# Performance work log

Hardware: AMD Instinct MI355X
Metric: run time of the kernel (lower is better)

The kernel has to match this reference:

```python
import jax, jax.numpy as jnp
import numpy as np

N_NODES = 100000
N_EDGES = 1600000
DK = 32
OUT_DIM = 32


def setup_inputs() -> dict:
    key = jax.random.key(0)
    ks = jax.random.split(key, 7)
    X = jax.random.normal(ks[0], (N_NODES, DK), dtype=jnp.float32)
    K = jax.random.normal(ks[1], (N_NODES, DK), dtype=jnp.float32)
    V = jax.random.normal(ks[2], (N_NODES, DK), dtype=jnp.float32)
    # output projection (nn.Dense(out_dim)) params
    W_o = jax.random.normal(ks[3], (DK, OUT_DIM), dtype=jnp.float32) / np.sqrt(DK)
    b_o = jnp.zeros((OUT_DIM,), dtype=jnp.float32)
    # sparsity descriptor td: edge list, dst sorted so segment ops see sorted ids
    src = jax.random.randint(ks[4], (N_EDGES,), 0, N_NODES, dtype=jnp.int32)
    dst = jnp.sort(jax.random.randint(ks[5], (N_EDGES,), 0, N_NODES, dtype=jnp.int32))
    return {"X": X, "K": K, "V": V, "W_o": W_o, "b_o": b_o,
            "src": src, "dst": dst, "num_seg": N_NODES}


def reference(X, K, V, W_o, b_o, src, dst, num_seg):
    dk = X.shape[-1]
    # per-edge attention logits: <Q[dst], K[src]> / dk  -> (E,)
    scores = jnp.einsum('ed,ed->e', jnp.take(X, dst, axis=0),
                        jnp.take(K, src, axis=0)) / dk
    # segment (per-neighborhood) softmax over edges sharing a dst node
    seg_max = jax.ops.segment_max(scores, dst, num_segments=num_seg,
                                  indices_are_sorted=True)
    e = jnp.exp(scores - jnp.take(seg_max, dst))
    denom = jax.ops.segment_sum(e, dst, num_segments=num_seg,
                                indices_are_sorted=True)
    alpha = e / jnp.take(denom, dst)  # (E,)
    # weighted aggregation of values, scattered back to nodes -> (N, dk)
    agg = jax.ops.segment_sum(alpha[:, None] * jnp.take(V, src, axis=0), dst,
                              num_segments=num_seg, indices_are_sorted=True)
    # output projection W_o
    return agg @ W_o + b_o
```

## Files before the change

### kernel.cpp

```cpp
#include <hip/hip_runtime.h>
#include <math.h>

#define DK 32
#define OUT_DIM 32

typedef float    f32x4 __attribute__((ext_vector_type(4)));
typedef _Float16 h2    __attribute__((ext_vector_type(2)));
typedef _Float16 h8    __attribute__((ext_vector_type(8)));

#if __has_builtin(__builtin_amdgcn_fdot2)
#define FDOT2(a, b, c) __builtin_amdgcn_fdot2((a), (b), (c), false)
#else
#define FDOT2(a, b, c) ((c) + (float)(a).x * (float)(b).x + (float)(a).y * (float)(b).y)
#endif

#if __has_builtin(__builtin_amdgcn_exp2f)
#define EXP2F(x) __builtin_amdgcn_exp2f(x)
#else
#define EXP2F(x) exp2f(x)
#endif

__device__ __forceinline__ h2 as_h2(unsigned u) {
    union { unsigned u; h2 h; } v; v.u = u; return v.h;
}
__device__ __forceinline__ unsigned as_u32(h2 h) {
    union { unsigned u; h2 h; } v; v.h = h; return v.u;
}
__device__ __forceinline__ h2 shfl_xor_h2(h2 v, int m) {
    union { unsigned u; h2 h; } x; x.h = v;
    x.u = (unsigned)__shfl_xor((int)x.u, m);
    return x.h;
}

__global__ void prep_kernel(const int* __restrict__ dst,
                            const float4* __restrict__ K4,
                            const float4* __restrict__ V4,
                            int E, int N,
                            int* __restrict__ row_ptr,
                            uint4* __restrict__ KVH) {
    const int t  = blockIdx.x * blockDim.x + threadIdx.x;
    const int e0 = t * 4;
    if (e0 < E) {
        int cur[4];
        if (e0 + 4 <= E) {
            const int4 dd = *(const int4*)(dst + e0);
            cur[0] = dd.x; cur[1] = dd.y; cur[2] = dd.z; cur[3] = dd.w;
        } else {
#pragma unroll
            for (int k = 0; k < 4; ++k)
                cur[k] = (e0 + k < E) ? dst[e0 + k] : 0;
        }
        int prev = (e0 == 0) ? -1 : dst[e0 - 1];
#pragma unroll
        for (int k = 0; k < 4; ++k) {
            const int ee = e0 + k;
            if (ee < E) {
                for (int j = prev + 1; j <= cur[k]; ++j) row_ptr[j] = ee;
                if (ee == E - 1)
                    for (int j = cur[k] + 1; j <= N; ++j) row_ptr[j] = E;
                prev = cur[k];
            }
        }
    }
    if (t < N * 8) {
        const float4 kf = K4[t];
        const float4 vf = V4[t];
        h2 k01, k23, v01, v23;
        k01.x = (_Float16)kf.x;  k01.y = (_Float16)kf.y;
        k23.x = (_Float16)kf.z;  k23.y = (_Float16)kf.w;
        v01.x = (_Float16)vf.x;  v01.y = (_Float16)vf.y;
        v23.x = (_Float16)vf.z;  v23.y = (_Float16)vf.w;
        uint4 o;
        o.x = as_u32(k01); o.y = as_u32(k23); o.z = as_u32(v01); o.w = as_u32(v23);
        KVH[t] = o;
    }
}

__global__ void build_row_ptr_kernel(const int* __restrict__ dst, int E, int N,
                                     int* __restrict__ row_ptr) {
    int e = blockIdx.x * blockDim.x + threadIdx.x;
    if (e >= E) return;
    int cur  = dst[e];
    int prev = (e == 0) ? -1 : dst[e - 1];
    for (int j = prev + 1; j <= cur; ++j) row_ptr[j] = e;
    if (e == E - 1) {
        for (int j = cur + 1; j <= N; ++j) row_ptr[j] = E;
    }
}

__global__ __launch_bounds__(256) void gat_fused_kernel(
    const float* __restrict__ X, const uint4* __restrict__ KV,
    const float* __restrict__ Wo, const float* __restrict__ bo,
    const int* __restrict__ src, const int* __restrict__ row_ptr,
    float* __restrict__ out, int N) {

    __shared__ uint4 s_part[16 * 17];

    const int tid  = threadIdx.x;
    const int w    = tid >> 6;
    const int lane = tid & 63;
    const int g    = lane >> 3;
    const int c    = lane & 7;

    const int n_blk = blockIdx.x * 16;
    const int n_w   = n_blk + w * 4;

    const int rpv = row_ptr[min(n_w + min(lane, 4), N)];

    const float4* X4 = (const float4*)X;
    unsigned* part32 = (unsigned*)s_part;
    const float scale = 0.03125f * 1.44269504f;

    int beg[4], en[4], cap[4], e[4];
#pragma unroll
    for (int i = 0; i < 4; ++i) {
        beg[i] = __builtin_amdgcn_readlane(rpv, i);
        en[i]  = __builtin_amdgcn_readlane(rpv, i + 1);
        cap[i] = max(en[i] - 1, 0);
        e[i]   = beg[i];
    }

    h2 q01[4], q23[4];
#pragma unroll
    for (int i = 0; i < 4; ++i) {
        const float4 qf = X4[min(n_w + i, N - 1) * 8 + c];
        q01[i].x = (_Float16)(qf.x * scale);
        q01[i].y = (_Float16)(qf.y * scale);
        q23[i].x = (_Float16)(qf.z * scale);
        q23[i].y = (_Float16)(qf.w * scale);
    }

    float l[4] = {0.0f, 0.0f, 0.0f, 0.0f};
    h2 a01[4], a23[4];
#pragma unroll
    for (int i = 0; i < 4; ++i) { a01[i] = (h2)0; a23[i] = (h2)0; }

    auto ldsrc = [&](int o, int* s) {
#pragma unroll
        for (int i = 0; i < 4; ++i) s[i] = src[min(e[i] + o + g, cap[i])];
    };
    auto ldkv = [&](const int* s, uint4* B) {
#pragma unroll
        for (int i = 0; i < 4; ++i) B[i] = KV[s[i] * 8 + c];
    };
    auto step = [&](const uint4* B) {
        float p[4];
#pragma unroll
        for (int i = 0; i < 4; ++i)
            p[i] = FDOT2(as_h2(B[i].y), q23[i], FDOT2(as_h2(B[i].x), q01[i], 0.0f));
#pragma unroll
        for (int i = 0; i < 4; ++i) p[i] += __shfl_xor(p[i], 1);
#pragma unroll
        for (int i = 0; i < 4; ++i) p[i] += __shfl_xor(p[i], 2);
#pragma unroll
        for (int i = 0; i < 4; ++i) p[i] += __shfl_xor(p[i], 4);
#pragma unroll
        for (int i = 0; i < 4; ++i) {
            const float wt = (e[i] + g < en[i]) ? EXP2F(p[i]) : 0.0f;
            l[i] += wt;
            h2 wh; wh.x = (_Float16)wt; wh.y = wh.x;
            a01[i] += wh * as_h2(B[i].z);
            a23[i] += wh * as_h2(B[i].w);
        }
    };
    auto nexists = [&]() {
        return (e[0] + 8 < en[0]) || (e[1] + 8 < en[1]) ||
               (e[2] + 8 < en[2]) || (e[3] + 8 < en[3]);
    };
    auto adv = [&]() {
#pragma unroll
        for (int i = 0; i < 4; ++i) e[i] += 8;
    };

    const bool any0 = (e[0] < en[0]) || (e[1] < en[1]) ||
                      (e[2] < en[2]) || (e[3] < en[3]);
    if (any0) {
        int s0[4], s1[4], s2[4], sCA[4], sAB[4], sBC[4];
        uint4 B0[4], B1[4], B2[4];
        ldsrc(0, s0);  ldsrc(8, s1);  ldsrc(16, s2);  ldsrc(24, sCA);
        ldkv(s0, B0);  ldkv(s1, B1);  ldkv(s2, B2);

        for (;;) {
            bool mn = nexists();
            step(B0);
            ldkv(sCA, B0);
            ldsrc(32, sAB);
            adv();
            if (!mn) break;
            mn = nexists();
            step(B1);
            ldkv(sAB, B1);
            ldsrc(32, sBC);
            adv();
            if (!mn) break;
            mn = nexists();
            step(B2);
            ldkv(sBC, B2);
            ldsrc(32, sCA);
            adv();
            if (!mn) break;
        }
    }

#pragma unroll
    for (int i = 0; i < 4; ++i) {
        l[i]   += __shfl_xor(l[i], 8);
        a01[i] += shfl_xor_h2(a01[i], 8);
        a23[i] += shfl_xor_h2(a23[i], 8);
        l[i] += __shfl_xor(l[i], 16);
        l[i] += __shfl_xor(l[i], 32);
        const float inv = (en[i] > beg[i]) ? (1.0f / l[i]) : 0.0f;
        h2 iv; iv.x = (_Float16)inv; iv.y = iv.x;
        a01[i] *= iv;  a23[i] *= iv;
    }

    if ((g & 1) == 0) {
        const int p = g >> 1;
#pragma unroll
        for (int i = 0; i < 4; ++i) {
            const int off = (w * 4 + i) * 68 + p * 16 + c * 2;
            part32[off]     = as_u32(a01[i]);
            part32[off + 1] = as_u32(a23[i]);
        }
    }

    __syncthreads();

    if (w == 0) {
        const int quad = lane >> 4;
        const int col  = lane & 15;

        union BF { h8 v; _Float16 u[8]; };
        BF bf0, bf1;
#pragma unroll
        for (int j2 = 0; j2 < 8; ++j2) {
            bf0.u[j2] = (_Float16)Wo[(quad * 8 + j2) * OUT_DIM + col];
            bf1.u[j2] = (_Float16)Wo[(quad * 8 + j2) * OUT_DIM + 16 + col];
        }
        const float bias0 = bo[col];
        const float bias1 = bo[16 + col];

        union AF { uint4 u; h8 v; };
        f32x4 C0 = {bias0, bias0, bias0, bias0};
        f32x4 C1 = {bias1, bias1, bias1, bias1};
#pragma unroll
        for (int cc = 0; cc < 4; ++cc) {
            AF a;
            a.u = s_part[col * 17 + cc * 4 + quad];
            C0 = __builtin_amdgcn_mfma_f32_16x16x32_f16(a.v, bf0.v, C0, 0, 0, 0);
            C1 = __builtin_amdgcn_mfma_f32_16x16x32_f16(a.v, bf1.v, C1, 0, 0, 0);
        }
#pragma unroll
        for (int r = 0; r < 4; ++r) {
            const int n = n_blk + quad * 4 + r;
            if (n < N) {
                out[n * OUT_DIM + col]      = C0[r];
                out[n * OUT_DIM + 16 + col] = C1[r];
            }
        }
    }
}

__global__ __launch_bounds__(256) void gat_node_f32_kernel(
    const float* __restrict__ X, const float* __restrict__ Km,
    const float* __restrict__ Vm, const float* __restrict__ Wo,
    const float* __restrict__ bo, const int* __restrict__ src,
    const int* __restrict__ row_ptr, float* __restrict__ out, int N) {
    const int tid  = threadIdx.x;
    const int wave = tid >> 6;
    const int lane = tid & 63;
    const int g    = lane >> 3;
    const int c    = lane & 7;
    const int j    = lane & 31;
    const int half = lane >> 5;
    const int n = blockIdx.x * 4 + wave;
    if (n >= N) return;
    const int begin = row_ptr[n];
    const int end   = row_ptr[n + 1];
    const float4* X4 = (const float4*)X;
    const float4* K4 = (const float4*)Km;
    const float4* V4 = (const float4*)Vm;
    const float4 q4 = X4[n * 8 + c];
    float  l   = 0.0f;
    float4 acc = make_float4(0.0f, 0.0f, 0.0f, 0.0f);
    for (int e0 = begin; e0 < end; e0 += 16) {
        const int  ea = e0 + g;
        const int  eb = ea + 8;
        const bool va = ea < end;
        const bool vb = eb < end;
        const int sa = src[min(ea, end - 1)];
        const int sb = src[min(eb, end - 1)];
        const float4 ka  = K4[sa * 8 + c];
        const float4 kb  = K4[sb * 8 + c];
        const float4 vva = V4[sa * 8 + c];
        const float4 vvb = V4[sb * 8 + c];
        float pa = fmaf(ka.x, q4.x, fmaf(ka.y, q4.y, fmaf(ka.z, q4.z, ka.w * q4.w)));
        float pb = fmaf(kb.x, q4.x, fmaf(kb.y, q4.y, fmaf(kb.z, q4.z, kb.w * q4.w)));
        pa += __shfl_xor(pa, 1);  pb += __shfl_xor(pb, 1);
        pa += __shfl_xor(pa, 2);  pb += __shfl_xor(pb, 2);
        pa += __shfl_xor(pa, 4);  pb += __shfl_xor(pb, 4);
        const float wa = va ? __expf(pa * 0.03125f) : 0.0f;
        const float wb = vb ? __expf(pb * 0.03125f) : 0.0f;
        l += wa + wb;
        acc.x = fmaf(wa, vva.x, acc.x);  acc.y = fmaf(wa, vva.y, acc.y);
        acc.z = fmaf(wa, vva.z, acc.z);  acc.w = fmaf(wa, vva.w, acc.w);
        acc.x = fmaf(wb, vvb.x, acc.x);  acc.y = fmaf(wb, vvb.y, acc.y);
        acc.z = fmaf(wb, vvb.z, acc.z);  acc.w = fmaf(wb, vvb.w, acc.w);
    }
#pragma unroll
    for (int m = 8; m <= 32; m <<= 1) {
        l     += __shfl_xor(l, m);
        acc.x += __shfl_xor(acc.x, m);
        acc.y += __shfl_xor(acc.y, m);
        acc.z += __shfl_xor(acc.z, m);
        acc.w += __shfl_xor(acc.w, m);
    }
    const float inv = (end > begin) ? (1.0f / l) : 0.0f;
    float ag[4] = {acc.x, acc.y, acc.z, acc.w};
    float s = 0.0f;
#pragma unroll
    for (int k = 0; k < 32; ++k) {
        const float a = __int_as_float(
            __builtin_amdgcn_readlane(__float_as_int(ag[k & 3]), k >> 2));
        s = fmaf(a, Wo[k * OUT_DIM + j], s);
    }
    if (half == 0) {
        out[n * OUT_DIM + j] = fmaf(s, inv, bo[j]);
    }
}

extern "C" void kernel_launch(void* const* d_in, const int* in_sizes, int n_in,
                              void* d_out, int out_size, void* d_ws, size_t ws_size,
                              hipStream_t stream) {
    const float* X  = (const float*)d_in[0];
    const float* Km = (const float*)d_in[1];
    const float* Vm = (const float*)d_in[2];
    const float* Wo = (const float*)d_in[3];
    const float* bo = (const float*)d_in[4];
    const int* src  = (const int*)d_in[5];
    const int* dst  = (const int*)d_in[6];

    const int N = in_sizes[0] / DK;
    const int E = in_sizes[5];

    int* row_ptr = (int*)d_ws;
    const size_t kv_off = (((size_t)(N + 1) * 4) + 127) & ~(size_t)127;
    unsigned* KV = (unsigned*)((char*)d_ws + kv_off);
    const size_t need = kv_off + (size_t)N * DK * 4;
    float* out = (float*)d_out;

    const int tb = 256;

    if (ws_size >= need) {
        const int nE4   = (E + 3) / 4;
        const int total = N * 8;
        const int prep_n = (nE4 > total) ? nE4 : total;
        prep_kernel<<<(prep_n + tb - 1) / tb, tb, 0, stream>>>(
            dst, (const float4*)Km, (const float4*)Vm, E, N,
            row_ptr, (uint4*)KV);
        const int grid = (N + 15) / 16;
        gat_fused_kernel<<<grid, 256, 0, stream>>>(X, (const uint4*)KV, Wo, bo,
                                                   src, row_ptr, out, N);
    } else {
        build_row_ptr_kernel<<<(E + tb - 1) / tb, tb, 0, stream>>>(dst, E, N, row_ptr);
        const int grid = (N + 3) / 4;
        gat_node_f32_kernel<<<grid, 256, 0, stream>>>(X, Km, Vm, Wo, bo,
                                                      src, row_ptr, out, N);
    }
}
```

Baseline: 136.3 us.

## Assign one wave per node and replace rotating prefetch pipeline with upfront loads

The fused attention kernel changes from each wave handling four nodes with a three-stage rotating src/KV prefetch pipeline to each wave handling one node. Blocks grow to 512 threads covering 8 nodes, and unused LDS rows for the MFMA projection are zero-filled so half the tile is padding. The per-node loop issues up to four gathers upfront, then loads the rest serially without prefetch. This is meant to raise wave-level parallelism and cut register pressure and inter-node imbalance, at the cost of more waves, wasted MFMA rows and less latency hiding for high-degree nodes.

```diff
diff --git a/kernel.cpp b/kernel.cpp
--- a/kernel.cpp
+++ b/kernel.cpp
@@ -88,7 +88,7 @@
     }
 }
 
-__global__ __launch_bounds__(256) void gat_fused_kernel(
+__global__ __launch_bounds__(512) void gat_fused_kernel(
     const float* __restrict__ X, const uint4* __restrict__ KV,
     const float* __restrict__ Wo, const float* __restrict__ bo,
     const int* __restrict__ src, const int* __restrict__ row_ptr,
@@ -102,126 +102,81 @@
     const int g    = lane >> 3;
     const int c    = lane & 7;
 
-    const int n_blk = blockIdx.x * 16;
-    const int n_w   = n_blk + w * 4;
-
-    const int rpv = row_ptr[min(n_w + min(lane, 4), N)];
-
-    const float4* X4 = (const float4*)X;
-    unsigned* part32 = (unsigned*)s_part;
+    const int n_blk = blockIdx.x * 8;
+    const int n     = n_blk + w;
+
+    if (tid < 136) {
+        uint4 z; z.x = 0; z.y = 0; z.z = 0; z.w = 0;
+        s_part[136 + tid] = z;
+    }
+
+    const int B    = __builtin_amdgcn_readfirstlane(row_ptr[min(n, N)]);
+    const int En   = __builtin_amdgcn_readfirstlane(row_ptr[min(n + 1, N)]);
+    const int deg  = En - B;
+    const int dcap = max(En - 1, 0);
+    const int T    = (deg + 7) >> 3;
+
     const float scale = 0.03125f * 1.44269504f;
-
-    int beg[4], en[4], cap[4], e[4];
-#pragma unroll
-    for (int i = 0; i < 4; ++i) {
-        beg[i] = __builtin_amdgcn_readlane(rpv, i);
-        en[i]  = __builtin_amdgcn_readlane(rpv, i + 1);
-        cap[i] = max(en[i] - 1, 0);
-        e[i]   = beg[i];
-    }
-
-    h2 q01[4], q23[4];
-#pragma unroll
-    for (int i = 0; i < 4; ++i) {
-        const float4 qf = X4[min(n_w + i, N - 1) * 8 + c];
-        q01[i].x = (_Float16)(qf.x * scale);
-        q01[i].y = (_Float16)(qf.y * scale);
-        q23[i].x = (_Float16)(qf.z * scale);
-        q23[i].y = (_Float16)(qf.w * scale);
-    }
-
-    float l[4] = {0.0f, 0.0f, 0.0f, 0.0f};
-    h2 a01[4], a23[4];
-#pragma unroll
-    for (int i = 0; i < 4; ++i) { a01[i] = (h2)0; a23[i] = (h2)0; }
-
-    auto ldsrc = [&](int o, int* s) {
-#pragma unroll
-        for (int i = 0; i < 4; ++i) s[i] = src[min(e[i] + o + g, cap[i])];
+    const float4 qf = ((const float4*)X)[min(n, N - 1) * 8 + c];
+    h2 q01, q23;
+    q01.x = (_Float16)(qf.x * scale);  q01.y = (_Float16)(qf.y * scale);
+    q23.x = (_Float16)(qf.z * scale);  q23.y = (_Float16)(qf.w * scale);
+
+    float l = 0.0f;
+    h2 a01 = (h2)0, a23 = (h2)0;
+
+    auto step = [&](const uint4& Bf, int t) {
+        float p = FDOT2(as_h2(Bf.y), q23, FDOT2(as_h2(Bf.x), q01, 0.0f));
+        p += __shfl_xor(p, 1);
+        p += __shfl_xor(p, 2);
+        p += __shfl_xor(p, 4);
+        const float wt = (t * 8 + g < deg) ? EXP2F(p) : 0.0f;
+        l += wt;
+        h2 wh; wh.x = (_Float16)wt; wh.y = wh.x;
+        a01 += wh * as_h2(Bf.z);
+        a23 += wh * as_h2(Bf.w);
     };
-    auto ldkv = [&](const int* s, uint4* B) {
-#pragma unroll
-        for (int i = 0; i < 4; ++i) B[i] = KV[s[i] * 8 + c];
-    };
-    auto step = [&](const uint4* B) {
-        float p[4];
-#pragma unroll
-        for (int i = 0; i < 4; ++i)
-            p[i] = FDOT2(as_h2(B[i].y), q23[i], FDOT2(as_h2(B[i].x), q01[i], 0.0f));
-#pragma unroll
-        for (int i = 0; i < 4; ++i) p[i] += __shfl_xor(p[i], 1);
-#pragma unroll
-        for (int i = 0; i < 4; ++i) p[i] += __shfl_xor(p[i], 2);
-#pragma unroll
-        for (int i = 0; i < 4; ++i) p[i] += __shfl_xor(p[i], 4);
-#pragma unroll
-        for (int i = 0; i < 4; ++i) {
-            const float wt = (e[i] + g < en[i]) ? EXP2F(p[i]) : 0.0f;
-            l[i] += wt;
-            h2 wh; wh.x = (_Float16)wt; wh.y = wh.x;
-            a01[i] += wh * as_h2(B[i].z);
-            a23[i] += wh * as_h2(B[i].w);
-        }
-    };
-    auto nexists = [&]() {
-        return (e[0] + 8 < en[0]) || (e[1] + 8 < en[1]) ||
-               (e[2] + 8 < en[2]) || (e[3] + 8 < en[3]);
-    };
-    auto adv = [&]() {
-#pragma unroll
-        for (int i = 0; i < 4; ++i) e[i] += 8;
-    };
-
-    const bool any0 = (e[0] < en[0]) || (e[1] < en[1]) ||
-                      (e[2] < en[2]) || (e[3] < en[3]);
-    if (any0) {
-        int s0[4], s1[4], s2[4], sCA[4], sAB[4], sBC[4];
-        uint4 B0[4], B1[4], B2[4];
-        ldsrc(0, s0);  ldsrc(8, s1);  ldsrc(16, s2);  ldsrc(24, sCA);
-        ldkv(s0, B0);  ldkv(s1, B1);  ldkv(s2, B2);
-
-        for (;;) {
-            bool mn = nexists();
-            step(B0);
-            ldkv(sCA, B0);
-            ldsrc(32, sAB);
-            adv();
-            if (!mn) break;
-            mn = nexists();
-            step(B1);
-            ldkv(sAB, B1);
-            ldsrc(32, sBC);
-            adv();
-            if (!mn) break;
-            mn = nexists();
-            step(B2);
-            ldkv(sBC, B2);
-            ldsrc(32, sCA);
-            adv();
-            if (!mn) break;
-        }
-    }
-
-#pragma unroll
-    for (int i = 0; i < 4; ++i) {
-        l[i]   += __shfl_xor(l[i], 8);
-        a01[i] += shfl_xor_h2(a01[i], 8);
-        a23[i] += shfl_xor_h2(a23[i], 8);
-        l[i] += __shfl_xor(l[i], 16);
-        l[i] += __shfl_xor(l[i], 32);
-        const float inv = (en[i] > beg[i]) ? (1.0f / l[i]) : 0.0f;
-        h2 iv; iv.x = (_Float16)inv; iv.y = iv.x;
-        a01[i] *= iv;  a23[i] *= iv;
-    }
+
+    if (T > 0) {
+        const int base = B + g;
+        const int s0 = src[min(base, dcap)];
+        int s1 = 0, s2 = 0, s3 = 0;
+        if (T > 1) s1 = src[min(base + 8,  dcap)];
+        if (T > 2) s2 = src[min(base + 16, dcap)];
+        if (T > 3) s3 = src[min(base + 24, dcap)];
+        uint4 P0, P1, P2, P3;
+        P0 = KV[s0 * 8 + c];
+        if (T > 1) P1 = KV[s1 * 8 + c];
+        if (T > 2) P2 = KV[s2 * 8 + c];
+        if (T > 3) P3 = KV[s3 * 8 + c];
+
+        step(P0, 0);
+        if (T > 1) step(P1, 1);
+        if (T > 2) step(P2, 2);
+        if (T > 3) step(P3, 3);
+
+        for (int t = 4; t < T; ++t) {
+            const int sx = src[min(B + t * 8 + g, dcap)];
+            const uint4 Px = KV[sx * 8 + c];
+            step(Px, t);
+        }
+    }
+
+    l   += __shfl_xor(l, 8);
+    a01 += shfl_xor_h2(a01, 8);
+    a23 += shfl_xor_h2(a23, 8);
+    l += __shfl_xor(l, 16);
+    l += __shfl_xor(l, 32);
+
+    const float inv = (deg > 0) ? (1.0f / l) : 0.0f;
+    h2 iv; iv.x = (_Float16)inv; iv.y = iv.x;
+    a01 *= iv;  a23 *= iv;
 
     if ((g & 1) == 0) {
-        const int p = g >> 1;
-#pragma unroll
-        for (int i = 0; i < 4; ++i) {
-            const int off = (w * 4 + i) * 68 + p * 16 + c * 2;
-            part32[off]     = as_u32(a01[i]);
-            part32[off + 1] = as_u32(a23[i]);
-        }
+        unsigned* part32 = (unsigned*)s_part;
+        const int off = w * 68 + (g >> 1) * 16 + c * 2;
+        part32[off]     = as_u32(a01);
+        part32[off + 1] = as_u32(a23);
     }
 
     __syncthreads();
@@ -250,12 +205,14 @@
             C0 = __builtin_amdgcn_mfma_f32_16x16x32_f16(a.v, bf0.v, C0, 0, 0, 0);
             C1 = __builtin_amdgcn_mfma_f32_16x16x32_f16(a.v, bf1.v, C1, 0, 0, 0);
         }
-#pragma unroll
-        for (int r = 0; r < 4; ++r) {
-            const int n = n_blk + quad * 4 + r;
-            if (n < N) {
-                out[n * OUT_DIM + col]      = C0[r];
-                out[n * OUT_DIM + 16 + col] = C1[r];
+        if (quad < 2) {
+#pragma unroll
+            for (int r = 0; r < 4; ++r) {
+                const int n2 = n_blk + quad * 4 + r;
+                if (n2 < N) {
+                    out[n2 * OUT_DIM + col]      = C0[r];
+                    out[n2 * OUT_DIM + 16 + col] = C1[r];
+                }
             }
         }
     }
@@ -358,8 +315,8 @@
         prep_kernel<<<(prep_n + tb - 1) / tb, tb, 0, stream>>>(
             dst, (const float4*)Km, (const float4*)Vm, E, N,
             row_ptr, (uint4*)KV);
-        const int grid = (N + 15) / 16;
-        gat_fused_kernel<<<grid, 256, 0, stream>>>(X, (const uint4*)KV, Wo, bo,
+        const int grid = (N + 7) / 8;
+        gat_fused_kernel<<<grid, 512, 0, stream>>>(X, (const uint4*)KV, Wo, bo,
                                                    src, row_ptr, out, N);
     } else {
         build_row_ptr_kernel<<<(E + tb - 1) / tb, tb, 0, stream>>>(dst, E, N, row_ptr);
```

After: 141.6 us. 3.9% more time.
